# Kernel tuning notes

Hardware: AMD Instinct MI355X
Metric: run time of the kernel (lower is better)

Reference implementation:

```python
import jax, jax.numpy as jnp
import numpy as np

L, T, C, H, K = 512, 96, 150, 150, 5

def conv1d(x, w):
    # x: (N, W, Cin), w: (K, Cin, Cout) -> (N, W, Cout), stride 1, SAME padding
    return jax.lax.conv_general_dilated(x, w, (1,), 'SAME',
                                        dimension_numbers=('NWC', 'WIO', 'NWC'))

def gru_layer(xs, Wi, bi, Wh):
    # xs: (B, T, Cin); conv acts over the leading B axis (treated as spatial by flax Conv)
    B = xs.shape[0]
    Hf = Wh.shape[1]
    # dense_i is independent per timestep: batch it over T in one conv
    xi = conv1d(jnp.swapaxes(xs, 0, 1), Wi) + bi  # (T, B, 3H)

    def step(h, xi_t):
        hh = conv1d(h[None], Wh)[0]               # (B, 3H)
        xr, xz, xn = jnp.split(xi_t, 3, axis=-1)
        hr, hz, hn = jnp.split(hh, 3, axis=-1)
        r = jax.nn.sigmoid(xr + hr)
        z = jax.nn.sigmoid(xz + hz)
        n = jnp.tanh(xn + r * hn)
        h_new = (1.0 - z) * n + z * h
        return h_new, h_new

    h0 = jnp.zeros((B, Hf), xs.dtype)
    _, ys = jax.lax.scan(step, h0, xi)            # ys: (T, B, H)
    return jnp.swapaxes(ys, 0, 1)                 # (B, T, H)

def setup_inputs() -> dict:
    key = jax.random.key(0)
    ks = jax.random.split(key, 6)
    s = 0.05  # keep gate pre-activations in a sane range
    return {
        'xs':   jax.random.normal(ks[0], (L, T, C), jnp.float32),
        'W_i0': jax.random.normal(ks[1], (K, C, 3 * H), jnp.float32) * s,
        'b_i0': jnp.zeros((3 * H,), jnp.float32),
        'W_h0': jax.random.normal(ks[2], (K, H, 3 * H), jnp.float32) * s,
        'W_i1': jax.random.normal(ks[3], (K, H, 3 * H), jnp.float32) * s,
        'b_i1': jnp.zeros((3 * H,), jnp.float32),
        'W_h1': jax.random.normal(ks[4], (K, H, 3 * H), jnp.float32) * s,
    }

def reference(xs, W_i0, b_i0, W_h0, W_i1, b_i1, W_h1):
    ys = gru_layer(xs, W_i0, b_i0, W_h0)
    ys = gru_layer(ys, W_i1, b_i1, W_h1)
    return ys
```

## Files before the change

### kernel.cpp

```cpp
#include <hip/hip_runtime.h>
#include <math.h>

#define LB     512
#define TSTEPS 96
#define CIN    150
#define HDIM   150
#define KW     5
#define CO3    450
#define NBT    16
#define NJT    15
#define BROWS  32
#define JW     10
#define NCH    15
#define CICH   10
#define HROWS  36
#define HPAD   152
#define CNTSTR 32
#define STITER 11

__device__ __forceinline__ float fsigmoid(float x) {
    return __builtin_amdgcn_rcpf(1.f + __expf(-x));
}
__device__ __forceinline__ float ftanh(float x) {
    return fmaf(2.f, __builtin_amdgcn_rcpf(1.f + __expf(-2.f * x)), -1.f);
}

__device__ __forceinline__ float h_load(const float* p) {
    return __hip_atomic_load(p, __ATOMIC_RELAXED, __HIP_MEMORY_SCOPE_AGENT);
}
__device__ __forceinline__ void h_store(float* p, float v) {
    __hip_atomic_store(p, v, __ATOMIC_RELAXED, __HIP_MEMORY_SCOPE_AGENT);
}

__global__ __launch_bounds__(256) void xi_conv_kernel(
    const float* __restrict__ src, long srcB, long srcT,
    const float* __restrict__ Wi, const float* __restrict__ bias,
    float* __restrict__ xi)
{
    __shared__ __align__(16) float xsh[CIN][20];
    const int b0  = blockIdx.x * 16;
    const int t   = blockIdx.y;
    const int tid = threadIdx.x;

    for (int idx = tid; idx < 20 * CIN; idx += 256) {
        int row = idx / CIN;
        int ci  = idx - row * CIN;
        int bp  = b0 + row - 2;
        float v = 0.f;
        if (bp >= 0 && bp < LB) v = src[(long)bp * srcB + (long)t * srcT + ci];
        xsh[ci][row] = v;
    }
    __syncthreads();

    if (tid < 225) {
        const int co = 2 * tid;
        float acc0[16], acc1[16];
        #pragma unroll
        for (int b = 0; b < 16; ++b) { acc0[b] = 0.f; acc1[b] = 0.f; }

        for (int ci = 0; ci < CIN; ++ci) {
            float4 a0 = *(const float4*)&xsh[ci][0];
            float4 a1 = *(const float4*)&xsh[ci][4];
            float4 a2 = *(const float4*)&xsh[ci][8];
            float4 a3 = *(const float4*)&xsh[ci][12];
            float4 a4 = *(const float4*)&xsh[ci][16];
            float xr[20];
            xr[0]=a0.x; xr[1]=a0.y; xr[2]=a0.z; xr[3]=a0.w;
            xr[4]=a1.x; xr[5]=a1.y; xr[6]=a1.z; xr[7]=a1.w;
            xr[8]=a2.x; xr[9]=a2.y; xr[10]=a2.z; xr[11]=a2.w;
            xr[12]=a3.x; xr[13]=a3.y; xr[14]=a3.z; xr[15]=a3.w;
            xr[16]=a4.x; xr[17]=a4.y; xr[18]=a4.z; xr[19]=a4.w;

            #pragma unroll
            for (int k = 0; k < KW; ++k) {
                const float2 w = *(const float2*)&Wi[((long)(k * CIN + ci)) * CO3 + co];
                #pragma unroll
                for (int b = 0; b < 16; ++b) {
                    float x = xr[b + k];
                    acc0[b] = fmaf(w.x, x, acc0[b]);
                    acc1[b] = fmaf(w.y, x, acc1[b]);
                }
            }
        }

        const float2 bia = *(const float2*)&bias[co];
        float* xo = xi + ((long)t * LB + b0) * CO3 + co;
        #pragma unroll
        for (int b = 0; b < 16; ++b) {
            float2 o; o.x = acc0[b] + bia.x; o.y = acc1[b] + bia.y;
            *(float2*)&xo[(long)b * CO3] = o;
        }
    }
}

__global__ __launch_bounds__(512, 1) void gru_seq_kernel(
    const float* __restrict__ Wh,
    const float* __restrict__ xi,
    float* __restrict__ ybase,
    long yT, long bS,
    int* __restrict__ cnt)
{
    __shared__ __align__(16) float hsh[HROWS][HPAD];
    __shared__ float part[NCH][BROWS][3 * JW];

    const int blk = blockIdx.x;
    const int bt  = blk / NJT;
    const int jt  = blk - bt * NJT;
    const int b0  = bt * BROWS;
    const int j0  = jt * JW;
    const int tid = threadIdx.x;

    const bool act = (tid < NCH * 3 * JW);
    const int  c   = tid % (3 * JW);
    const int  ch  = tid / (3 * JW);
    const int  g   = c / JW;
    const int  jl  = c - g * JW;
    const int  co  = g * HDIM + j0 + jl;
    const int  ci0 = ch * CICH;

    const bool gthr = (tid < BROWS * JW);
    const int  grow = tid / JW;
    const int  gj   = tid - grow * JW;

    float w[KW][CICH];
    if (act) {
        #pragma unroll
        for (int k = 0; k < KW; ++k)
            #pragma unroll
            for (int i = 0; i < CICH; ++i)
                w[k][i] = Wh[((long)(k * CIN + ci0 + i)) * CO3 + co];
    }

    for (int t = 0; t < TSTEPS; ++t) {
        if (t > 0 && tid < 3) {
            int x = bt - 1 + tid;
            if (x >= 0 && x < NBT) {
                const int tgt = NJT * t;
                while (__hip_atomic_load(&cnt[x * CNTSTR], __ATOMIC_RELAXED,
                                         __HIP_MEMORY_SCOPE_AGENT) < tgt)
                    __builtin_amdgcn_s_sleep(1);
            }
        }
        __syncthreads();

        float pxr = 0.f, pxz = 0.f, pxn = 0.f;
        if (gthr) {
            const float* xp = xi + ((long)t * LB + b0 + grow) * CO3 + j0 + gj;
            pxr = xp[0];
            pxz = xp[HDIM];
            pxn = xp[2 * HDIM];
        }

        if (t > 0) {
            const float* hsrc = ybase + (long)(t - 1) * yT;
            float v[STITER];
            int   rw[STITER], cv[STITER];
            bool  ok[STITER];
            #pragma unroll
            for (int it = 0; it < STITER; ++it) {
                int idx = tid + it * 512;
                int row = idx / CIN;
                int ci  = idx - row * CIN;
                int gr  = b0 - 2 + row;
                ok[it]  = (idx < HROWS * CIN) && (gr >= 0) && (gr < LB);
                int grc = gr < 0 ? 0 : (gr >= LB - 1 ? LB - 1 : gr);
                v[it]   = h_load(&hsrc[(long)grc * bS + ci]);
                rw[it]  = row; cv[it] = ci;
            }
            #pragma unroll
            for (int it = 0; it < STITER; ++it) {
                int idx = tid + it * 512;
                if (idx < HROWS * CIN)
                    hsh[rw[it]][cv[it]] = ok[it] ? v[it] : 0.f;
            }
        } else {
            #pragma unroll
            for (int it = 0; it < STITER; ++it) {
                int idx = tid + it * 512;
                if (idx < HROWS * CIN) hsh[idx / CIN][idx % CIN] = 0.f;
            }
        }
        __syncthreads();

        if (act) {
            float acc[BROWS];
            #pragma unroll
            for (int r = 0; r < BROWS; ++r) acc[r] = 0.f;
            #pragma unroll
            for (int p = 0; p < CICH / 2; ++p) {
                #pragma unroll
                for (int row = 0; row < HROWS; ++row) {
                    float2 h2 = *(const float2*)&hsh[row][ci0 + 2 * p];
                    #pragma unroll
                    for (int k = 0; k < KW; ++k) {
                        const int r = row - k;
                        if (r >= 0 && r < BROWS) {
                            acc[r] = fmaf(w[k][2 * p],     h2.x, acc[r]);
                            acc[r] = fmaf(w[k][2 * p + 1], h2.y, acc[r]);
                        }
                    }
                }
            }
            #pragma unroll
            for (int r = 0; r < BROWS; ++r) part[ch][r][c] = acc[r];
        }
        __syncthreads();

        if (gthr) {
            float hr = 0.f, hz = 0.f, hn = 0.f;
            #pragma unroll
            for (int s = 0; s < NCH; ++s) {
                hr += part[s][grow][gj];
                hz += part[s][grow][JW + gj];
                hn += part[s][grow][2 * JW + gj];
            }
            const int b = b0 + grow;
            float r  = fsigmoid(pxr + hr);
            float z  = fsigmoid(pxz + hz);
            float n  = ftanh(fmaf(r, hn, pxn));
            float hp = hsh[grow + 2][j0 + gj];
            h_store(&ybase[(long)t * yT + (long)b * bS + j0 + gj],
                    fmaf(z, hp - n, n));
        }
        __syncthreads();

        if (tid == 0)
            __hip_atomic_fetch_add(&cnt[bt * CNTSTR], 1, __ATOMIC_RELAXED,
                                   __HIP_MEMORY_SCOPE_AGENT);
    }
}

__global__ void zero_cnt_kernel(int* cnt) {
    for (int i = threadIdx.x; i < 2 * NBT * CNTSTR; i += 256) cnt[i] = 0;
}

extern "C" void kernel_launch(void* const* d_in, const int* in_sizes, int n_in,
                              void* d_out, int out_size, void* d_ws, size_t ws_size,
                              hipStream_t stream) {
    const float* xs  = (const float*)d_in[0];
    const float* Wi0 = (const float*)d_in[1];
    const float* bi0 = (const float*)d_in[2];
    const float* Wh0 = (const float*)d_in[3];
    const float* Wi1 = (const float*)d_in[4];
    const float* bi1 = (const float*)d_in[5];
    const float* Wh1 = (const float*)d_in[6];
    float* out = (float*)d_out;

    int*   cnt = (int*)d_ws;
    float* xi  = (float*)((char*)d_ws + 4096);
    float* ys0 = xi + (size_t)TSTEPS * LB * CO3;

    hipLaunchKernelGGL(zero_cnt_kernel, dim3(1), dim3(256), 0, stream, cnt);

    dim3 gxi(32, TSTEPS);

    hipLaunchKernelGGL(xi_conv_kernel, gxi, dim3(256), 0, stream,
                       xs, (long)(TSTEPS * CIN), (long)CIN, Wi0, bi0, xi);
    {
        const float* Wh = Wh0; const float* xip = xi; float* yb = ys0;
        long yT = (long)LB * HDIM;
        long bS = (long)HDIM;
        int* c0 = cnt;
        void* args[] = { (void*)&Wh, (void*)&xip, (void*)&yb,
                         (void*)&yT, (void*)&bS, (void*)&c0 };
        hipLaunchCooperativeKernel((void*)gru_seq_kernel, dim3(NBT * NJT),
                                   dim3(512), args, 0, stream);
    }

    hipLaunchKernelGGL(xi_conv_kernel, gxi, dim3(256), 0, stream,
                       ys0, (long)HDIM, (long)(LB * HDIM), Wi1, bi1, xi);
    {
        const float* Wh = Wh1; const float* xip = xi; float* yb = out;
        long yT = (long)HDIM;
        long bS = (long)(TSTEPS * HDIM);
        int* c1 = cnt + NBT * CNTSTR;
        void* args[] = { (void*)&Wh, (void*)&xip, (void*)&yb,
                         (void*)&yT, (void*)&bS, (void*)&c1 };
        hipLaunchCooperativeKernel((void*)gru_seq_kernel, dim3(NBT * NJT),
                                   dim3(512), args, 0, stream);
    }
}
```

Baseline: 2.778 ms.

## Split halo rows from interior so the convolution overlaps the neighbour wait

Each block now waits only on its own batch tile's counter, then loads and convolves the 32 interior rows. Only after that does it wait on the neighbouring tiles and fetch the four halo rows, adding their contributions through a small extra partial-sum buffer. This moves the inter-block dependency wait off the critical path so it overlaps with interior compute. The cost is an extra barrier, a second small global load phase and additional shared memory.

```diff
diff --git a/kernel.cpp b/kernel.cpp
--- a/kernel.cpp
+++ b/kernel.cpp
@@ -16,7 +16,7 @@
 #define HROWS  36
 #define HPAD   152
 #define CNTSTR 32
-#define STITER 11
+#define PARTR  33
 
 __device__ __forceinline__ float fsigmoid(float x) {
     return __builtin_amdgcn_rcpf(1.f + __expf(-x));
@@ -101,7 +101,8 @@
     int* __restrict__ cnt)
 {
     __shared__ __align__(16) float hsh[HROWS][HPAD];
-    __shared__ float part[NCH][BROWS][3 * JW];
+    __shared__ float part[NCH][PARTR][3 * JW];
+    __shared__ float parth[NCH][4][33];
 
     const int blk = blockIdx.x;
     const int bt  = blk / NJT;
@@ -121,6 +122,8 @@
     const bool gthr = (tid < BROWS * JW);
     const int  grow = tid / JW;
     const int  gj   = tid - grow * JW;
+    const bool bdry = gthr && (grow < 2 || grow >= 30);
+    const int  rrb  = (grow < 2) ? grow : grow - 28;
 
     float w[KW][CICH];
     if (act) {
@@ -132,14 +135,11 @@
     }
 
     for (int t = 0; t < TSTEPS; ++t) {
-        if (t > 0 && tid < 3) {
-            int x = bt - 1 + tid;
-            if (x >= 0 && x < NBT) {
-                const int tgt = NJT * t;
-                while (__hip_atomic_load(&cnt[x * CNTSTR], __ATOMIC_RELAXED,
-                                         __HIP_MEMORY_SCOPE_AGENT) < tgt)
-                    __builtin_amdgcn_s_sleep(1);
-            }
+        if (t > 0 && tid == 0) {
+            const int tgt = NJT * t;
+            while (__hip_atomic_load(&cnt[bt * CNTSTR], __ATOMIC_RELAXED,
+                                     __HIP_MEMORY_SCOPE_AGENT) < tgt)
+                __builtin_amdgcn_s_sleep(1);
         }
         __syncthreads();
 
@@ -150,35 +150,27 @@
             pxz = xp[HDIM];
             pxn = xp[2 * HDIM];
         }
-
         if (t > 0) {
             const float* hsrc = ybase + (long)(t - 1) * yT;
-            float v[STITER];
-            int   rw[STITER], cv[STITER];
-            bool  ok[STITER];
-            #pragma unroll
-            for (int it = 0; it < STITER; ++it) {
+            float v[10];
+            #pragma unroll
+            for (int it = 0; it < 10; ++it) {
                 int idx = tid + it * 512;
-                int row = idx / CIN;
-                int ci  = idx - row * CIN;
-                int gr  = b0 - 2 + row;
-                ok[it]  = (idx < HROWS * CIN) && (gr >= 0) && (gr < LB);
-                int grc = gr < 0 ? 0 : (gr >= LB - 1 ? LB - 1 : gr);
-                v[it]   = h_load(&hsrc[(long)grc * bS + ci]);
-                rw[it]  = row; cv[it] = ci;
-            }
-            #pragma unroll
-            for (int it = 0; it < STITER; ++it) {
+                int ci2 = (idx < BROWS * CIN) ? idx : (BROWS * CIN - 1);
+                int row = ci2 / CIN, ci = ci2 - row * CIN;
+                v[it] = h_load(&hsrc[(long)(b0 + row) * bS + ci]);
+            }
+            #pragma unroll
+            for (int it = 0; it < 10; ++it) {
                 int idx = tid + it * 512;
-                if (idx < HROWS * CIN)
-                    hsh[rw[it]][cv[it]] = ok[it] ? v[it] : 0.f;
+                if (idx < BROWS * CIN) {
+                    int row = idx / CIN, ci = idx - row * CIN;
+                    hsh[row + 2][ci] = v[it];
+                }
             }
         } else {
-            #pragma unroll
-            for (int it = 0; it < STITER; ++it) {
-                int idx = tid + it * 512;
-                if (idx < HROWS * CIN) hsh[idx / CIN][idx % CIN] = 0.f;
-            }
+            for (int idx = tid; idx < HROWS * CIN; idx += 512)
+                hsh[idx / CIN][idx % CIN] = 0.f;
         }
         __syncthreads();
 
@@ -189,7 +181,7 @@
             #pragma unroll
             for (int p = 0; p < CICH / 2; ++p) {
                 #pragma unroll
-                for (int row = 0; row < HROWS; ++row) {
+                for (int row = 2; row < 34; ++row) {
                     float2 h2 = *(const float2*)&hsh[row][ci0 + 2 * p];
                     #pragma unroll
                     for (int k = 0; k < KW; ++k) {
@@ -204,6 +196,52 @@
             #pragma unroll
             for (int r = 0; r < BROWS; ++r) part[ch][r][c] = acc[r];
         }
+
+        if (t > 0 && tid < 2) {
+            const int x = bt + (tid ? 1 : -1);
+            if (x >= 0 && x < NBT) {
+                const int tgt = NJT * t;
+                while (__hip_atomic_load(&cnt[x * CNTSTR], __ATOMIC_RELAXED,
+                                         __HIP_MEMORY_SCOPE_AGENT) < tgt)
+                    __builtin_amdgcn_s_sleep(1);
+            }
+        }
+        __syncthreads();
+        if (t > 0 && tid < 300) {
+            const float* hsrc = ybase + (long)(t - 1) * yT;
+            int e0 = tid, e1 = tid + 300;
+            int h0r = e0 / CIN, c0_ = e0 - h0r * CIN;
+            int h1r = e1 / CIN, c1_ = e1 - h1r * CIN;
+            int s0 = (h0r < 2) ? h0r : h0r + 32;
+            int s1 = (h1r < 2) ? h1r : h1r + 32;
+            int g0 = b0 - 2 + s0, g1 = b0 - 2 + s1;
+            int g0c = g0 < 0 ? 0 : (g0 > LB - 1 ? LB - 1 : g0);
+            int g1c = g1 < 0 ? 0 : (g1 > LB - 1 ? LB - 1 : g1);
+            float va = h_load(&hsrc[(long)g0c * bS + c0_]);
+            float vb = h_load(&hsrc[(long)g1c * bS + c1_]);
+            hsh[s0][c0_] = (g0 >= 0 && g0 < LB) ? va : 0.f;
+            hsh[s1][c1_] = (g1 >= 0 && g1 < LB) ? vb : 0.f;
+        }
+        __syncthreads();
+
+        if (act) {
+            float a4[4] = {0.f, 0.f, 0.f, 0.f};
+            #pragma unroll
+            for (int p = 0; p < CICH / 2; ++p) {
+                float2 h0 = *(const float2*)&hsh[0][ci0 + 2 * p];
+                float2 h1 = *(const float2*)&hsh[1][ci0 + 2 * p];
+                float2 h34 = *(const float2*)&hsh[34][ci0 + 2 * p];
+                float2 h35 = *(const float2*)&hsh[35][ci0 + 2 * p];
+                a4[0] = fmaf(w[0][2*p], h0.x,  fmaf(w[0][2*p+1], h0.y,  a4[0]));
+                a4[0] = fmaf(w[1][2*p], h1.x,  fmaf(w[1][2*p+1], h1.y,  a4[0]));
+                a4[1] = fmaf(w[0][2*p], h1.x,  fmaf(w[0][2*p+1], h1.y,  a4[1]));
+                a4[2] = fmaf(w[4][2*p], h34.x, fmaf(w[4][2*p+1], h34.y, a4[2]));
+                a4[3] = fmaf(w[3][2*p], h34.x, fmaf(w[3][2*p+1], h34.y, a4[3]));
+                a4[3] = fmaf(w[4][2*p], h35.x, fmaf(w[4][2*p+1], h35.y, a4[3]));
+            }
+            #pragma unroll
+            for (int rr = 0; rr < 4; ++rr) parth[ch][rr][c] = a4[rr];
+        }
         __syncthreads();
 
         if (gthr) {
@@ -213,6 +251,14 @@
                 hr += part[s][grow][gj];
                 hz += part[s][grow][JW + gj];
                 hn += part[s][grow][2 * JW + gj];
+            }
+            if (bdry) {
+                #pragma unroll
+                for (int s = 0; s < NCH; ++s) {
+                    hr += parth[s][rrb][gj];
+                    hz += parth[s][rrb][JW + gj];
+                    hn += parth[s][rrb][2 * JW + gj];
+                }
             }
             const int b = b0 + grow;
             float r  = fsigmoid(pxr + hr);
```

After: 3.112 ms. 1.12x slower.

## Split GRU recurrent conv rows across two thread groups with 1024-thread blocks

Applied to the files above, without the earlier changes.

Doubles the recurrent GRU block to 1024 threads. Each half computes 16 of the 32 batch rows of the hidden-state conv, which halves the per-thread serial FMA chain and the accumulator registers in the per-step critical path. The staging loop is adjusted for the larger block, and the partial-sum buffer gains a padding row. The cost is more waves per CU and more register pressure under launch bounds (1024,4), and each half redundantly loads 4 overlapping halo rows.

```diff
diff --git a/kernel.cpp b/kernel.cpp
--- a/kernel.cpp
+++ b/kernel.cpp
@@ -16,7 +16,8 @@
 #define HROWS  36
 #define HPAD   152
 #define CNTSTR 32
-#define STITER 11
+#define PARTR  33
+#define STIT   6
 
 __device__ __forceinline__ float fsigmoid(float x) {
     return __builtin_amdgcn_rcpf(1.f + __expf(-x));
@@ -93,7 +94,7 @@
     }
 }
 
-__global__ __launch_bounds__(512, 1) void gru_seq_kernel(
+__global__ __launch_bounds__(1024, 4) void gru_seq_kernel(
     const float* __restrict__ Wh,
     const float* __restrict__ xi,
     float* __restrict__ ybase,
@@ -101,7 +102,7 @@
     int* __restrict__ cnt)
 {
     __shared__ __align__(16) float hsh[HROWS][HPAD];
-    __shared__ float part[NCH][BROWS][3 * JW];
+    __shared__ float part[NCH][PARTR][3 * JW];
 
     const int blk = blockIdx.x;
     const int bt  = blk / NJT;
@@ -110,13 +111,16 @@
     const int j0  = jt * JW;
     const int tid = threadIdx.x;
 
-    const bool act = (tid < NCH * 3 * JW);
-    const int  c   = tid % (3 * JW);
-    const int  ch  = tid / (3 * JW);
+    const int  rg  = tid >> 9;
+    const int  tl  = tid & 511;
+    const bool act = (tl < NCH * 3 * JW);
+    const int  c   = tl % (3 * JW);
+    const int  ch  = tl / (3 * JW);
     const int  g   = c / JW;
     const int  jl  = c - g * JW;
     const int  co  = g * HDIM + j0 + jl;
     const int  ci0 = ch * CICH;
+    const int  rbase = rg * 16;
 
     const bool gthr = (tid < BROWS * JW);
     const int  grow = tid / JW;
@@ -153,56 +157,52 @@
 
         if (t > 0) {
             const float* hsrc = ybase + (long)(t - 1) * yT;
-            float v[STITER];
-            int   rw[STITER], cv[STITER];
-            bool  ok[STITER];
-            #pragma unroll
-            for (int it = 0; it < STITER; ++it) {
-                int idx = tid + it * 512;
-                int row = idx / CIN;
-                int ci  = idx - row * CIN;
+            float v[STIT];
+            int   rw[STIT], cv[STIT];
+            bool  ok[STIT];
+            #pragma unroll
+            for (int it = 0; it < STIT; ++it) {
+                int idx = tid + it * 1024;
+                int idc = (idx < HROWS * CIN) ? idx : (HROWS * CIN - 1);
+                int row = idc / CIN, ci = idc - row * CIN;
                 int gr  = b0 - 2 + row;
                 ok[it]  = (idx < HROWS * CIN) && (gr >= 0) && (gr < LB);
-                int grc = gr < 0 ? 0 : (gr >= LB - 1 ? LB - 1 : gr);
+                int grc = gr < 0 ? 0 : (gr > LB - 1 ? LB - 1 : gr);
                 v[it]   = h_load(&hsrc[(long)grc * bS + ci]);
                 rw[it]  = row; cv[it] = ci;
             }
             #pragma unroll
-            for (int it = 0; it < STITER; ++it) {
-                int idx = tid + it * 512;
-                if (idx < HROWS * CIN)
+            for (int it = 0; it < STIT; ++it) {
+                if (tid + it * 1024 < HROWS * CIN)
                     hsh[rw[it]][cv[it]] = ok[it] ? v[it] : 0.f;
             }
         } else {
-            #pragma unroll
-            for (int it = 0; it < STITER; ++it) {
-                int idx = tid + it * 512;
-                if (idx < HROWS * CIN) hsh[idx / CIN][idx % CIN] = 0.f;
-            }
+            for (int idx = tid; idx < HROWS * CIN; idx += 1024)
+                hsh[idx / CIN][idx % CIN] = 0.f;
         }
         __syncthreads();
 
         if (act) {
-            float acc[BROWS];
-            #pragma unroll
-            for (int r = 0; r < BROWS; ++r) acc[r] = 0.f;
+            float acc[16];
+            #pragma unroll
+            for (int r = 0; r < 16; ++r) acc[r] = 0.f;
             #pragma unroll
             for (int p = 0; p < CICH / 2; ++p) {
                 #pragma unroll
-                for (int row = 0; row < HROWS; ++row) {
-                    float2 h2 = *(const float2*)&hsh[row][ci0 + 2 * p];
+                for (int row = 0; row < 20; ++row) {
+                    float2 h2 = *(const float2*)&hsh[rbase + row][ci0 + 2 * p];
                     #pragma unroll
                     for (int k = 0; k < KW; ++k) {
-                        const int r = row - k;
-                        if (r >= 0 && r < BROWS) {
-                            acc[r] = fmaf(w[k][2 * p],     h2.x, acc[r]);
-                            acc[r] = fmaf(w[k][2 * p + 1], h2.y, acc[r]);
+                        const int rl = row - k;
+                        if (rl >= 0 && rl < 16) {
+                            acc[rl] = fmaf(w[k][2 * p],     h2.x, acc[rl]);
+                            acc[rl] = fmaf(w[k][2 * p + 1], h2.y, acc[rl]);
                         }
                     }
                 }
             }
             #pragma unroll
-            for (int r = 0; r < BROWS; ++r) part[ch][r][c] = acc[r];
+            for (int rl = 0; rl < 16; ++rl) part[ch][rbase + rl][c] = acc[rl];
         }
         __syncthreads();
 
@@ -264,7 +264,7 @@
         void* args[] = { (void*)&Wh, (void*)&xip, (void*)&yb,
                          (void*)&yT, (void*)&bS, (void*)&c0 };
         hipLaunchCooperativeKernel((void*)gru_seq_kernel, dim3(NBT * NJT),
-                                   dim3(512), args, 0, stream);
+                                   dim3(1024), args, 0, stream);
     }
 
     hipLaunchKernelGGL(xi_conv_kernel, gxi, dim3(256), 0, stream,
@@ -277,6 +277,6 @@
         void* args[] = { (void*)&Wh, (void*)&xip, (void*)&yb,
                          (void*)&yT, (void*)&bS, (void*)&c1 };
         hipLaunchCooperativeKernel((void*)gru_seq_kernel, dim3(NBT * NJT),
-                                   dim3(512), args, 0, stream);
-    }
-}
+                                   dim3(1024), args, 0, stream);
+    }
+}
```

After: 3.377 ms. 21.6% more time.
